# Kernel tuning notes

Measured on AMD Instinct MI355X. Metric: run time of the kernel, lower is better.

## Reference

```python
import jax, jax.numpy as jnp
import numpy as np

MARGIN = 1.0


def setup_inputs() -> dict:
    key = jax.random.key(0)
    k1, k2 = jax.random.split(key)
    B, D, K = 2048, 256, 8
    scores = jax.random.normal(k1, (B, D), dtype=jnp.float32)
    pos_indices = jax.random.randint(k2, (B, K), 0, D, dtype=jnp.int64)
    return {"scores": scores, "pos_indices": pos_indices, "num_developers": D}


def reference(scores, pos_indices, num_developers):
    B, D = scores.shape
    # boolean positive mask per sample (duplicate indices collapse like a set)
    pos_mask = jnp.zeros((B, D), dtype=scores.dtype)
    pos_mask = pos_mask.at[jnp.arange(B)[:, None], pos_indices].set(1.0)
    neg_mask = 1.0 - pos_mask
    # all-pairs hinge: relu(s_neg - s_pos + margin), masked to (neg, pos) pairs
    # diff[b, n, p] = scores[b, n] - scores[b, p] + margin
    diff = scores[:, :, None] - scores[:, None, :] + MARGIN
    pair_mask = neg_mask[:, :, None] * pos_mask[:, None, :]
    loss_sum = jnp.sum(jax.nn.relu(diff) * pair_mask)
    num_pairs = jnp.sum(pair_mask)
    # original returns 0.0 when there are no (pos, neg) pairs
    return jnp.where(num_pairs > 0, loss_sum / jnp.maximum(num_pairs, 1.0), 0.0)
```

## Files before the change

kernel.cpp:

```cpp
#include <hip/hip_runtime.h>

#define TPB 256
#define MAXB 512
#define MAXPOS 64

__global__ void mlrl_main(const float* __restrict__ scores,
                          const int* __restrict__ idx,
                          const int* __restrict__ ndev,
                          int total_scores, int total_idx,
                          double* __restrict__ partial_loss,
                          double* __restrict__ partial_pairs) {
    const int D = *ndev;
    const int B = total_scores / D;
    const int K = total_idx / B;

    __shared__ float sh_pos[MAXPOS];
    __shared__ int   sh_cnt;

    double loss  = 0.0;
    double pairs = 0.0;

    for (int b = blockIdx.x; b < B; b += gridDim.x) {
        if (threadIdx.x == 0) sh_cnt = 0;
        __syncthreads();

        const int*   row_idx = idx    + (long)b * K;
        const float* row_s   = scores + (long)b * D;

        for (int d = threadIdx.x; d < D; d += blockDim.x) {
            bool is_pos = false;
            for (int k = 0; k < K; ++k) is_pos |= (row_idx[k] == d);
            if (is_pos) {
                int p = atomicAdd(&sh_cnt, 1);
                if (p < MAXPOS) sh_pos[p] = row_s[d];
            }
        }
        __syncthreads();
        const int P = sh_cnt;

        for (int d = threadIdx.x; d < D; d += blockDim.x) {
            bool is_pos = false;
            for (int k = 0; k < K; ++k) is_pos |= (row_idx[k] == d);
            if (!is_pos) {
                const float s = row_s[d];
                for (int p = 0; p < P; ++p) {
                    float v = s - sh_pos[p] + 1.0f;
                    if (v > 0.0f) loss += (double)v;
                }
            }
        }
        if (threadIdx.x == 0) pairs += (double)(D - P) * (double)P;
        __syncthreads();
    }

    __shared__ double red[TPB];
    red[threadIdx.x] = loss;
    __syncthreads();
    for (int s = TPB / 2; s > 0; s >>= 1) {
        if (threadIdx.x < s) red[threadIdx.x] += red[threadIdx.x + s];
        __syncthreads();
    }
    if (threadIdx.x == 0) {
        partial_loss[blockIdx.x]  = red[0];
        partial_pairs[blockIdx.x] = pairs;
    }
}

__global__ void mlrl_finalize(const double* __restrict__ partial_loss,
                              const double* __restrict__ partial_pairs,
                              int n, float* __restrict__ out) {
    __shared__ double sl[TPB];
    __shared__ double sp[TPB];
    double l = 0.0, p = 0.0;
    for (int i = threadIdx.x; i < n; i += blockDim.x) {
        l += partial_loss[i];
        p += partial_pairs[i];
    }
    sl[threadIdx.x] = l;
    sp[threadIdx.x] = p;
    __syncthreads();
    for (int s = TPB / 2; s > 0; s >>= 1) {
        if (threadIdx.x < s) {
            sl[threadIdx.x] += sl[threadIdx.x + s];
            sp[threadIdx.x] += sp[threadIdx.x + s];
        }
        __syncthreads();
    }
    if (threadIdx.x == 0) {
        double L = sl[0], P = sp[0];
        out[0] = (P > 0.0) ? (float)(L / (P < 1.0 ? 1.0 : P)) : 0.0f;
    }
}

extern "C" void kernel_launch(void* const* d_in, const int* in_sizes, int n_in,
                              void* d_out, int out_size, void* d_ws, size_t ws_size,
                              hipStream_t stream) {
    const float* scores = (const float*)d_in[0];
    const int*   idx    = (const int*)d_in[1];
    const int*   ndev   = (const int*)d_in[2];
    float* out = (float*)d_out;

    const int total_scores = in_sizes[0];
    const int total_idx    = in_sizes[1];

    int nblocks = MAXB;
    size_t need = (size_t)nblocks * 2 * sizeof(double);
    if (ws_size < need) {
        nblocks = (int)(ws_size / (2 * sizeof(double)));
        if (nblocks < 1) nblocks = 1;
    }
    double* partial_loss  = (double*)d_ws;
    double* partial_pairs = partial_loss + nblocks;

    mlrl_main<<<nblocks, TPB, 0, stream>>>(scores, idx, ndev,
                                           total_scores, total_idx,
                                           partial_loss, partial_pairs);
    mlrl_finalize<<<1, TPB, 0, stream>>>(partial_loss, partial_pairs, nblocks, out);
}
```

Before: 68.76 us.

## Use fp32 accumulation, shared index dedup, wave-shuffle reductions, one block per row

Loads each row's K indices into shared memory once, dedups them there and gathers the positive scores directly, replacing the atomic counting pass. Per-thread accumulation switches from double to float, block reductions use wave shuffles, and partials are packed as float2. The grid becomes total_scores/256 blocks, one per row here, instead of 512. Float accumulation avoids slow fp64 adds but may lose accuracy relative to the double-based sum.

Measured after the change: 66.57 us. 3.2% less time.

```diff
diff --git a/kernel.cpp b/kernel.cpp
--- a/kernel.cpp
+++ b/kernel.cpp
@@ -1,93 +1,96 @@
 #include <hip/hip_runtime.h>
 
 #define TPB 256
-#define MAXB 512
-#define MAXPOS 64
+#define MAXK 64
 
-__global__ void mlrl_main(const float* __restrict__ scores,
-                          const int* __restrict__ idx,
-                          const int* __restrict__ ndev,
-                          int total_scores, int total_idx,
-                          double* __restrict__ partial_loss,
-                          double* __restrict__ partial_pairs) {
+__global__ __launch_bounds__(TPB) void mlrl_main(
+        const float* __restrict__ scores,
+        const int* __restrict__ idx,
+        const int* __restrict__ ndev,
+        int total_scores, int total_idx,
+        float2* __restrict__ partials) {
     const int D = *ndev;
     const int B = total_scores / D;
     const int K = total_idx / B;
 
-    __shared__ float sh_pos[MAXPOS];
-    __shared__ int   sh_cnt;
+    __shared__ int   sh_idx[MAXK];
+    __shared__ float sh_pos[MAXK];
+    __shared__ int   sh_valid[MAXK];
 
-    double loss  = 0.0;
-    double pairs = 0.0;
+    float loss  = 0.0f;
+    float pairs = 0.0f;
 
     for (int b = blockIdx.x; b < B; b += gridDim.x) {
-        if (threadIdx.x == 0) sh_cnt = 0;
+        const long row = (long)b * D;
+
+        if (threadIdx.x < K) sh_idx[threadIdx.x] = idx[(long)b * K + threadIdx.x];
+        __syncthreads();
+        if (threadIdx.x < K) {
+            const int my = sh_idx[threadIdx.x];
+            int valid = 1;
+            for (int j = 0; j < (int)threadIdx.x; ++j)
+                if (sh_idx[j] == my) valid = 0;
+            sh_valid[threadIdx.x] = valid;
+            sh_pos[threadIdx.x]   = scores[row + my];
+        }
         __syncthreads();
 
-        const int*   row_idx = idx    + (long)b * K;
-        const float* row_s   = scores + (long)b * D;
+        int P = 0;
+        for (int k = 0; k < K; ++k) P += sh_valid[k];
 
         for (int d = threadIdx.x; d < D; d += blockDim.x) {
             bool is_pos = false;
-            for (int k = 0; k < K; ++k) is_pos |= (row_idx[k] == d);
-            if (is_pos) {
-                int p = atomicAdd(&sh_cnt, 1);
-                if (p < MAXPOS) sh_pos[p] = row_s[d];
-            }
-        }
-        __syncthreads();
-        const int P = sh_cnt;
-
-        for (int d = threadIdx.x; d < D; d += blockDim.x) {
-            bool is_pos = false;
-            for (int k = 0; k < K; ++k) is_pos |= (row_idx[k] == d);
+            for (int k = 0; k < K; ++k) is_pos |= (sh_idx[k] == d);
             if (!is_pos) {
-                const float s = row_s[d];
-                for (int p = 0; p < P; ++p) {
-                    float v = s - sh_pos[p] + 1.0f;
-                    if (v > 0.0f) loss += (double)v;
+                const float s = scores[row + d] + 1.0f;
+                for (int k = 0; k < K; ++k) {
+                    if (sh_valid[k]) {
+                        float v = s - sh_pos[k];
+                        loss += (v > 0.0f) ? v : 0.0f;
+                    }
                 }
             }
         }
-        if (threadIdx.x == 0) pairs += (double)(D - P) * (double)P;
+        if (threadIdx.x == 0) pairs += (float)((D - P) * P);
         __syncthreads();
     }
 
-    __shared__ double red[TPB];
-    red[threadIdx.x] = loss;
+    for (int off = 32; off > 0; off >>= 1) {
+        loss  += __shfl_down(loss,  off);
+        pairs += __shfl_down(pairs, off);
+    }
+    __shared__ float2 red[TPB / 64];
+    const int wave = threadIdx.x >> 6;
+    const int lane = threadIdx.x & 63;
+    if (lane == 0) red[wave] = make_float2(loss, pairs);
     __syncthreads();
-    for (int s = TPB / 2; s > 0; s >>= 1) {
-        if (threadIdx.x < s) red[threadIdx.x] += red[threadIdx.x + s];
-        __syncthreads();
-    }
     if (threadIdx.x == 0) {
-        partial_loss[blockIdx.x]  = red[0];
-        partial_pairs[blockIdx.x] = pairs;
+        float2 acc = red[0];
+        for (int w = 1; w < TPB / 64; ++w) { acc.x += red[w].x; acc.y += red[w].y; }
+        partials[blockIdx.x] = acc;
     }
 }
 
-__global__ void mlrl_finalize(const double* __restrict__ partial_loss,
-                              const double* __restrict__ partial_pairs,
-                              int n, float* __restrict__ out) {
-    __shared__ double sl[TPB];
-    __shared__ double sp[TPB];
+__global__ __launch_bounds__(TPB) void mlrl_finalize(
+        const float2* __restrict__ partials, int n, float* __restrict__ out) {
     double l = 0.0, p = 0.0;
     for (int i = threadIdx.x; i < n; i += blockDim.x) {
-        l += partial_loss[i];
-        p += partial_pairs[i];
+        float2 v = partials[i];
+        l += (double)v.x;
+        p += (double)v.y;
     }
-    sl[threadIdx.x] = l;
-    sp[threadIdx.x] = p;
+    for (int off = 32; off > 0; off >>= 1) {
+        l += __shfl_down(l, off);
+        p += __shfl_down(p, off);
+    }
+    __shared__ double sl[TPB / 64], sp[TPB / 64];
+    const int wave = threadIdx.x >> 6;
+    const int lane = threadIdx.x & 63;
+    if (lane == 0) { sl[wave] = l; sp[wave] = p; }
     __syncthreads();
-    for (int s = TPB / 2; s > 0; s >>= 1) {
-        if (threadIdx.x < s) {
-            sl[threadIdx.x] += sl[threadIdx.x + s];
-            sp[threadIdx.x] += sp[threadIdx.x + s];
-        }
-        __syncthreads();
-    }
     if (threadIdx.x == 0) {
-        double L = sl[0], P = sp[0];
+        double L = 0.0, P = 0.0;
+        for (int w = 0; w < TPB / 64; ++w) { L += sl[w]; P += sp[w]; }
         out[0] = (P > 0.0) ? (float)(L / (P < 1.0 ? 1.0 : P)) : 0.0f;
     }
 }
@@ -103,17 +106,14 @@
     const int total_scores = in_sizes[0];
     const int total_idx    = in_sizes[1];
 
-    int nblocks = MAXB;
-    size_t need = (size_t)nblocks * 2 * sizeof(double);
-    if (ws_size < need) {
-        nblocks = (int)(ws_size / (2 * sizeof(double)));
-        if (nblocks < 1) nblocks = 1;
-    }
-    double* partial_loss  = (double*)d_ws;
-    double* partial_pairs = partial_loss + nblocks;
+    int nblocks = total_scores / 256;
+    if (nblocks < 1) nblocks = 1;
+    size_t need = (size_t)nblocks * sizeof(float2);
+    if (need > ws_size) nblocks = (int)(ws_size / sizeof(float2));
+
+    float2* partials = (float2*)d_ws;
 
     mlrl_main<<<nblocks, TPB, 0, stream>>>(scores, idx, ndev,
-                                           total_scores, total_idx,
-                                           partial_loss, partial_pairs);
-    mlrl_finalize<<<1, TPB, 0, stream>>>(partial_loss, partial_pairs, nblocks, out);
+                                           total_scores, total_idx, partials);
+    mlrl_finalize<<<1, TPB, 0, stream>>>(partials, nblocks, out);
 }
```
